# Kernel tuning notes

Hardware: AMD Instinct MI355X
Metric: run time of the kernel (lower is better)

Reference implementation:

```python
import jax, jax.numpy as jnp
import numpy as np

N = 50000   # nodes
E = 800000  # edges
F_IN, F_HID, F_OUT = 128, 96, 40


def setup_inputs() -> dict:
    key = jax.random.key(0)
    ks = jax.random.split(key, 9)
    x = jax.random.normal(ks[0], (N, F_IN), dtype=jnp.float32)
    edge_index = jax.random.randint(ks[1], (2, E), 0, N, dtype=jnp.int32)
    def lin(k, fi, fo):
        s = 1.0 / np.sqrt(fi)
        return jax.random.uniform(k, (fi, fo), jnp.float32, -s, s)
    W1 = lin(ks[2], F_IN, F_HID)
    b1 = jnp.zeros((F_HID,), jnp.float32)
    W2 = lin(ks[3], F_HID, F_HID)
    b2 = jnp.zeros((F_HID,), jnp.float32)
    Wout = lin(ks[4], F_HID, F_OUT)
    bout = jnp.zeros((F_OUT,), jnp.float32)
    return {"x": x, "edge_index": edge_index, "W1": W1, "b1": b1,
            "W2": W2, "b2": b2, "Wout": Wout, "bout": bout}


def _gcn_norm(edge_index, n):
    # add self-loops, symmetric degree normalization (PyG GCNConv default)
    loops = jnp.arange(n, dtype=edge_index.dtype)
    src = jnp.concatenate([edge_index[0], loops])
    dst = jnp.concatenate([edge_index[1], loops])
    deg = jax.ops.segment_sum(jnp.ones_like(dst, dtype=jnp.float32), dst,
                              num_segments=n)
    dinv = jnp.where(deg > 0, jax.lax.rsqrt(deg), 0.0)
    norm = dinv[src] * dinv[dst]   # [E+N]
    return src, dst, norm


def _gcn_layer(h, src, dst, norm, W, b, n):
    # linear transform, then normalized scatter-add aggregation, then bias
    h = h @ W                                 # [N, Fout]
    msg = h[src] * norm[:, None]              # gather + scale
    agg = jax.ops.segment_sum(msg, dst, num_segments=n)
    return agg + b


def reference(x, edge_index, W1, b1, W2, b2, Wout, bout):
    n = x.shape[0]
    src, dst, norm = _gcn_norm(edge_index, n)
    h = jax.nn.relu(_gcn_layer(x, src, dst, norm, W1, b1, n))
    h = jax.nn.relu(_gcn_layer(h, src, dst, norm, W2, b2, n))
    return h @ Wout + bout
```

## Files before the change

kernel.cpp:

```cpp
#include <hip/hip_runtime.h>
#include <hip/hip_fp16.h>

#define N_NODES 50000
#define N_EDGES 800000
#define F_INN   128
#define F_HID   96
#define F_OUTT  40

typedef _Float16 half8 __attribute__((ext_vector_type(8)));
typedef float    floatx4 __attribute__((ext_vector_type(4)));

template <int FI, typename TIN>
__device__ __forceinline__ void mfma_gemm_body(
        const TIN* __restrict__ X, const __half* __restrict__ BTg,
        float4* __restrict__ Th4, int n, int bx) {
    __shared__ __half BTl[96 * 136];
    __half* OUTl = BTl;
    int tid = threadIdx.x;
    {
        const int4* s = reinterpret_cast<const int4*>(BTg);
        int4* d = reinterpret_cast<int4*>(BTl);
        for (int i = tid; i < 96 * 136 / 8; i += 256) d[i] = s[i];
    }
    __syncthreads();

    int lane = tid & 63, w = tid >> 6;
    int lm = lane & 15, q = lane >> 4;
    int base = bx * 64 + w * 16;
    int node = base + lm;
    int nclamp = min(node, n - 1);
    const TIN* Xrow = X + (size_t)nclamp * FI;

    floatx4 cf[6];
    #pragma unroll
    for (int t = 0; t < 6; ++t) cf[t] = (floatx4){0.f, 0.f, 0.f, 0.f};

    constexpr int KS = FI / 32;
    #pragma unroll
    for (int ks = 0; ks < KS; ++ks) {
        half8 bv;
        if constexpr (sizeof(TIN) == 4) {
            const float4* xr = reinterpret_cast<const float4*>(Xrow + 32 * ks + q * 8);
            float4 f0 = xr[0], f1 = xr[1];
            union { half8 v; __half2 h[4]; } b;
            b.h[0] = __floats2half2_rn(f0.x, f0.y);
            b.h[1] = __floats2half2_rn(f0.z, f0.w);
            b.h[2] = __floats2half2_rn(f1.x, f1.y);
            b.h[3] = __floats2half2_rn(f1.z, f1.w);
            bv = b.v;
        } else {
            bv = *reinterpret_cast<const half8*>(Xrow + 32 * ks + q * 8);
        }
        #pragma unroll
        for (int t = 0; t < 6; ++t) {
            half8 a = *reinterpret_cast<const half8*>(
                &BTl[(t * 16 + lm) * 136 + q * 8 + 32 * ks]);
            cf[t] = __builtin_amdgcn_mfma_f32_16x16x32_f16(a, bv, cf[t], 0, 0, 0);
        }
    }

    __syncthreads();

    __half* orow = OUTl + (w * 16 + lm) * 104;
    #pragma unroll
    for (int t = 0; t < 6; ++t) {
        union { int2 i2; __half2 h[2]; } u;
        u.h[0] = __floats2half2_rn(cf[t][0], cf[t][1]);
        u.h[1] = __floats2half2_rn(cf[t][2], cf[t][3]);
        *reinterpret_cast<int2*>(&orow[t * 16 + q * 4]) = u.i2;
    }
    #pragma unroll
    for (int R = 0; R < 3; ++R) {
        int nl = lane >> 2, c = (lane & 3) + 4 * R;
        float4 v = *reinterpret_cast<const float4*>(&OUTl[(w * 16 + nl) * 104 + c * 8]);
        int gn = base + nl;
        if (gn < n) Th4[(size_t)gn * 12 + c] = v;
    }
}

__global__ __launch_bounds__(256) void count_gemm1_kernel(
        const int* __restrict__ dst, int* __restrict__ counts4, int* __restrict__ rank,
        int e, const float* __restrict__ X, const __half* __restrict__ BT1,
        float4* __restrict__ Th4, int n, int nCB) {
    if ((int)blockIdx.x < nCB) {
        int i = blockIdx.x * 512 + threadIdx.x;
        int j = i + 256;
        int di = 0, dj = 0, ri, rj;
        bool bi = i < e, bj = j < e;
        if (bi) di = dst[i];
        if (bj) dj = dst[j];
        if (bi) ri = atomicAdd(&counts4[di * 4 + (i & 3)], 1);
        if (bj) rj = atomicAdd(&counts4[dj * 4 + (j & 3)], 1);
        if (bi) rank[i] = ri;
        if (bj) rank[j] = rj;
    } else {
        mfma_gemm_body<F_INN, float>(X, BT1, Th4, n, blockIdx.x - nCB);
    }
}

template <int FI, typename TIN>
__global__ __launch_bounds__(256) void mfma_gemm_kernel(
        const TIN* __restrict__ X, const __half* __restrict__ BTg,
        float4* __restrict__ Th4, int n) {
    mfma_gemm_body<FI, TIN>(X, BTg, Th4, n, blockIdx.x);
}

__global__ void wt_kernel(const float* __restrict__ W1, const float* __restrict__ W2,
                          __half* __restrict__ BT1, __half* __restrict__ BT2) {
    int i = blockIdx.x * 256 + threadIdx.x;
    if (i < 96 * 128) {
        int j = i / 128, k = i - j * 128;
        BT1[j * 136 + k] = __float2half(W1[k * 96 + j]);
    } else if (i < 96 * 128 + 96 * 96) {
        int t = i - 96 * 128;
        int j = t / 96, k = t - j * 96;
        BT2[j * 136 + k] = __float2half(W2[k * 96 + j]);
    }
}

__global__ __launch_bounds__(1024) void scan_local_kernel(
        const int4* __restrict__ counts4, int* __restrict__ row_start,
        float* __restrict__ dinv, int* __restrict__ blk_sums, int n) {
    __shared__ int wave_sums[16];
    int tid = threadIdx.x, lane = tid & 63, wid = tid >> 6;
    int i = blockIdx.x * 1024 + tid;
    int v = 0;
    if (i < n) {
        int4 c = counts4[i];
        v = c.x + c.y + c.z + c.w;
    }
    int val = v;
    #pragma unroll
    for (int off = 1; off < 64; off <<= 1) {
        int u = __shfl_up(val, off, 64);
        if (lane >= off) val += u;
    }
    if (lane == 63) wave_sums[wid] = val;
    __syncthreads();
    if (wid == 0) {
        int w = (lane < 16) ? wave_sums[lane] : 0;
        #pragma unroll
        for (int off = 1; off < 16; off <<= 1) {
            int u = __shfl_up(w, off, 64);
            if (lane >= off) w += u;
        }
        if (lane < 16) wave_sums[lane] = w;
    }
    __syncthreads();
    int excl = ((wid == 0) ? 0 : wave_sums[wid - 1]) + (val - v);
    if (i < n) {
        row_start[i] = excl;
        dinv[i] = rsqrtf((float)(v + 1));
    }
    if (tid == 0) blk_sums[blockIdx.x] = wave_sums[15];
}

__global__ __launch_bounds__(1024) void scan_apply_kernel(
        int* __restrict__ row_start, const int* __restrict__ blk_sums,
        const int4* __restrict__ counts4, int4* __restrict__ base4, int n, int nblk) {
    __shared__ int s_my, s_tot;
    int tid = threadIdx.x;
    if (tid < 64) {
        int v = (tid < nblk) ? blk_sums[tid] : 0;
        int val = v;
        #pragma unroll
        for (int off = 1; off < 64; off <<= 1) {
            int u = __shfl_up(val, off, 64);
            if (tid >= off) val += u;
        }
        if (tid == (int)blockIdx.x) s_my = val - v;
        if (tid == 63) s_tot = val;
    }
    __syncthreads();
    int i = blockIdx.x * 1024 + tid;
    if (i < n) {
        int4 c = counts4[i];
        int b = row_start[i] + s_my;
        row_start[i] = b;
        base4[i] = make_int4(b, b + c.x, b + c.x + c.y, b + c.x + c.y + c.z);
    }
    if (blockIdx.x == 0 && tid == 0) row_start[n] = s_tot;
}

__global__ void fill_csr_kernel(const int* __restrict__ src, const int* __restrict__ dst,
                                const int* __restrict__ rank, const int* __restrict__ base4,
                                int* __restrict__ csr_src, int e) {
    int i = blockIdx.x * blockDim.x + threadIdx.x;
    if (i >= e) return;
    csr_src[base4[dst[i] * 4 + (i & 3)] + rank[i]] = src[i];
}

__global__ __launch_bounds__(256) void agg_kernel(
        const __half2* __restrict__ T, const int* __restrict__ row_start,
        const int* __restrict__ csr_src, const float* __restrict__ dinv,
        const float* __restrict__ bias, __half2* __restrict__ H, int n) {
    int lane = threadIdx.x & 63;
    int node = __builtin_amdgcn_readfirstlane(blockIdx.x * 4 + (threadIdx.x >> 6));
    if (node >= n) return;
    int fl = min(lane, 47);

    float dn = dinv[node];
    float2 self = __half22float2(T[(size_t)node * 48 + fl]);
    float accx = dn * self.x, accy = dn * self.y;

    int idx = row_start[node];
    int end = row_start[node + 1];
    for (; idx + 8 <= end; idx += 8) {
        int s[8];
        #pragma unroll
        for (int u = 0; u < 8; ++u) s[u] = csr_src[idx + u];
        float ws[8];
        #pragma unroll
        for (int u = 0; u < 8; ++u) ws[u] = dinv[s[u]];
        float2 f[8];
        #pragma unroll
        for (int u = 0; u < 8; ++u) f[u] = __half22float2(T[(size_t)s[u] * 48 + fl]);
        #pragma unroll
        for (int u = 0; u < 8; ++u) {
            accx = fmaf(ws[u], f[u].x, accx);
            accy = fmaf(ws[u], f[u].y, accy);
        }
    }
    for (; idx < end; ++idx) {
        int s = csr_src[idx];
        float w = dinv[s];
        float2 f = __half22float2(T[(size_t)s * 48 + fl]);
        accx = fmaf(w, f.x, accx);
        accy = fmaf(w, f.y, accy);
    }
    if (lane < 48) {
        float2 b = reinterpret_cast<const float2*>(bias)[lane];
        float ox = fmaxf(fmaf(dn, accx, b.x), 0.f);
        float oy = fmaxf(fmaf(dn, accy, b.y), 0.f);
        H[(size_t)node * 48 + lane] = __floats2half2_rn(ox, oy);
    }
}

__global__ __launch_bounds__(320) void gemm_out_kernel(
        const __half2* __restrict__ A, const float* __restrict__ W,
        const float* __restrict__ bias, float* __restrict__ C, int n) {
    __shared__ float Wlds[96 * 40];
    int tid = threadIdx.y * 10 + threadIdx.x;
    for (int i = tid; i < 96 * 10; i += 320)
        reinterpret_cast<float4*>(Wlds)[i] = reinterpret_cast<const float4*>(W)[i];
    __syncthreads();

    int j    = threadIdx.x * 4;
    int node = blockIdx.x * 32 + threadIdx.y;
    int nc   = min(node, n - 1);
    const __half2* Ah = A + (size_t)nc * 48;
    float4 acc = make_float4(0.f, 0.f, 0.f, 0.f);
    for (int k2 = 0; k2 < 48; k2 += 2) {
        float2 a01 = __half22float2(Ah[k2]);
        float2 a23 = __half22float2(Ah[k2 + 1]);
        int k = 2 * k2;
        float4 w0 = *reinterpret_cast<const float4*>(Wlds + (k + 0) * 40 + j);
        float4 w1 = *reinterpret_cast<const float4*>(Wlds + (k + 1) * 40 + j);
        float4 w2 = *reinterpret_cast<const float4*>(Wlds + (k + 2) * 40 + j);
        float4 w3 = *reinterpret_cast<const float4*>(Wlds + (k + 3) * 40 + j);
        acc.x += a01.x * w0.x + a01.y * w1.x + a23.x * w2.x + a23.y * w3.x;
        acc.y += a01.x * w0.y + a01.y * w1.y + a23.x * w2.y + a23.y * w3.y;
        acc.z += a01.x * w0.z + a01.y * w1.z + a23.x * w2.z + a23.y * w3.z;
        acc.w += a01.x * w0.w + a01.y * w1.w + a23.x * w2.w + a23.y * w3.w;
    }
    if (node < n) {
        float4 b = *reinterpret_cast<const float4*>(bias + j);
        acc.x += b.x; acc.y += b.y; acc.z += b.z; acc.w += b.w;
        *reinterpret_cast<float4*>(C + (size_t)node * 40 + j) = acc;
    }
}


extern "C" void kernel_launch(void* const* d_in, const int* in_sizes, int n_in,
                              void* d_out, int out_size, void* d_ws, size_t ws_size,
                              hipStream_t stream) {
    const float* x    = (const float*)d_in[0];
    const int*   ei   = (const int*)d_in[1];
    const float* W1   = (const float*)d_in[2];
    const float* b1   = (const float*)d_in[3];
    const float* W2   = (const float*)d_in[4];
    const float* b2   = (const float*)d_in[5];
    const float* Wout = (const float*)d_in[6];
    const float* bout = (const float*)d_in[7];
    float*       out  = (float*)d_out;

    const int* src = ei;
    const int* dst = ei + N_EDGES;

    char* ws = (char*)d_ws;
    size_t off = 0;
    auto alloc = [&](size_t bytes) {
        size_t o = off;
        off = (off + bytes + 511) & ~(size_t)511;
        return (void*)(ws + o);
    };
    int*     counts4   = (int*)    alloc((size_t)N_NODES * 4 * sizeof(int));
    int4*    base4     = (int4*)   alloc((size_t)N_NODES * sizeof(int4));
    int*     row_start = (int*)    alloc((N_NODES + 1) * sizeof(int));
    float*   dinv      = (float*)  alloc(N_NODES * sizeof(float));
    int*     blk_sums  = (int*)    alloc(64 * sizeof(int));
    int*     rank      = (int*)    alloc((size_t)N_EDGES * sizeof(int));
    int*     csr_src   = (int*)    alloc((size_t)N_EDGES * sizeof(int));
    __half*  BT1       = (__half*) alloc((size_t)96 * 136 * sizeof(__half));
    __half*  BT2       = (__half*) alloc((size_t)96 * 136 * sizeof(__half));
    __half2* Th        = (__half2*)alloc((size_t)N_NODES * 48 * sizeof(__half2));
    __half2* Hh        = (__half2*)alloc((size_t)N_NODES * 48 * sizeof(__half2));

    const int NSCAN = (N_NODES + 1023) / 1024;
    const int CB2   = (N_EDGES + 511) / 512;
    const int FB    = (N_EDGES + 255) / 256;
    const int GB    = (N_NODES + 63) / 64;

    hipMemsetAsync(counts4, 0, (size_t)N_NODES * 4 * sizeof(int), stream);
    wt_kernel<<<(96 * 128 + 96 * 96 + 255) / 256, 256, 0, stream>>>(W1, W2, BT1, BT2);

    count_gemm1_kernel<<<CB2 + GB, 256, 0, stream>>>(
        dst, counts4, rank, N_EDGES, x, BT1, (float4*)Th, N_NODES, CB2);

    scan_local_kernel<<<NSCAN, 1024, 0, stream>>>(
        (const int4*)counts4, row_start, dinv, blk_sums, N_NODES);
    scan_apply_kernel<<<NSCAN, 1024, 0, stream>>>(
        row_start, blk_sums, (const int4*)counts4, base4, N_NODES, NSCAN);
    fill_csr_kernel<<<FB, 256, 0, stream>>>(
        src, dst, rank, (const int*)base4, csr_src, N_EDGES);

    agg_kernel<<<(N_NODES + 3) / 4, 256, 0, stream>>>(
        Th, row_start, csr_src, dinv, b1, Hh, N_NODES);

    mfma_gemm_kernel<F_HID, __half><<<GB, 256, 0, stream>>>(
        (const __half*)Hh, BT2, (float4*)Th, N_NODES);
    agg_kernel<<<(N_NODES + 3) / 4, 256, 0, stream>>>(
        Th, row_start, csr_src, dinv, b2, Hh, N_NODES);

    gemm_out_kernel<<<(N_NODES + 31) / 32, dim3(10, 32), 0, stream>>>(
        Hh, Wout, bout, out, N_NODES);
}
```

Measured before the change: 230.1 us.

## Build CSR with atomic cursors instead of stored per-edge ranks

The count kernel no longer records a per-edge rank from its atomic; instead the scan writes per-node sub-bucket cursors and the fill kernel claims slots by atomically incrementing those cursors, with four edges per thread. This removes the rank array write and read (about 6.4 MB of traffic) at the cost of a second pass of atomics in the fill stage. Edge order within a node's row becomes nondeterministic, which can change floating-point summation order in aggregation.

```diff
diff --git a/kernel.cpp b/kernel.cpp
--- a/kernel.cpp
+++ b/kernel.cpp
@@ -79,20 +79,18 @@
 }
 
 __global__ __launch_bounds__(256) void count_gemm1_kernel(
-        const int* __restrict__ dst, int* __restrict__ counts4, int* __restrict__ rank,
+        const int* __restrict__ dst, int* __restrict__ counts4,
         int e, const float* __restrict__ X, const __half* __restrict__ BT1,
         float4* __restrict__ Th4, int n, int nCB) {
     if ((int)blockIdx.x < nCB) {
         int i = blockIdx.x * 512 + threadIdx.x;
         int j = i + 256;
-        int di = 0, dj = 0, ri, rj;
+        int di = 0, dj = 0;
         bool bi = i < e, bj = j < e;
         if (bi) di = dst[i];
         if (bj) dj = dst[j];
-        if (bi) ri = atomicAdd(&counts4[di * 4 + (i & 3)], 1);
-        if (bj) rj = atomicAdd(&counts4[dj * 4 + (j & 3)], 1);
-        if (bi) rank[i] = ri;
-        if (bj) rank[j] = rj;
+        if (bi) atomicAdd(&counts4[di * 4 + (i & 3)], 1);
+        if (bj) atomicAdd(&counts4[dj * 4 + (j & 3)], 1);
     } else {
         mfma_gemm_body<F_INN, float>(X, BT1, Th4, n, blockIdx.x - nCB);
     }
@@ -157,7 +155,7 @@
 
 __global__ __launch_bounds__(1024) void scan_apply_kernel(
         int* __restrict__ row_start, const int* __restrict__ blk_sums,
-        const int4* __restrict__ counts4, int4* __restrict__ base4, int n, int nblk) {
+        const int4* __restrict__ counts4, int4* __restrict__ cursor4, int n, int nblk) {
     __shared__ int s_my, s_tot;
     int tid = threadIdx.x;
     if (tid < 64) {
@@ -177,17 +175,30 @@
         int4 c = counts4[i];
         int b = row_start[i] + s_my;
         row_start[i] = b;
-        base4[i] = make_int4(b, b + c.x, b + c.x + c.y, b + c.x + c.y + c.z);
+        cursor4[i] = make_int4(b, b + c.x, b + c.x + c.y, b + c.x + c.y + c.z);
     }
     if (blockIdx.x == 0 && tid == 0) row_start[n] = s_tot;
 }
 
-__global__ void fill_csr_kernel(const int* __restrict__ src, const int* __restrict__ dst,
-                                const int* __restrict__ rank, const int* __restrict__ base4,
-                                int* __restrict__ csr_src, int e) {
-    int i = blockIdx.x * blockDim.x + threadIdx.x;
-    if (i >= e) return;
-    csr_src[base4[dst[i] * 4 + (i & 3)] + rank[i]] = src[i];
+__global__ __launch_bounds__(256) void fill_csr_kernel(
+        const int* __restrict__ src, const int* __restrict__ dst,
+        int* __restrict__ cursor4, int* __restrict__ csr_src, int e) {
+    int i0 = blockIdx.x * 1024 + threadIdx.x;
+    int sh = i0 & 3;
+    int d[4], s[4], p[4];
+    bool b[4];
+    #pragma unroll
+    for (int u = 0; u < 4; ++u) {
+        int i = i0 + u * 256;
+        b[u] = i < e;
+        if (b[u]) { d[u] = dst[i]; s[u] = src[i]; }
+    }
+    #pragma unroll
+    for (int u = 0; u < 4; ++u)
+        if (b[u]) p[u] = atomicAdd(&cursor4[d[u] * 4 + sh], 1);
+    #pragma unroll
+    for (int u = 0; u < 4; ++u)
+        if (b[u]) csr_src[p[u]] = s[u];
 }
 
 __global__ __launch_bounds__(256) void agg_kernel(
@@ -295,11 +306,10 @@
         return (void*)(ws + o);
     };
     int*     counts4   = (int*)    alloc((size_t)N_NODES * 4 * sizeof(int));
-    int4*    base4     = (int4*)   alloc((size_t)N_NODES * sizeof(int4));
+    int4*    cursor4   = (int4*)   alloc((size_t)N_NODES * sizeof(int4));
     int*     row_start = (int*)    alloc((N_NODES + 1) * sizeof(int));
     float*   dinv      = (float*)  alloc(N_NODES * sizeof(float));
     int*     blk_sums  = (int*)    alloc(64 * sizeof(int));
-    int*     rank      = (int*)    alloc((size_t)N_EDGES * sizeof(int));
     int*     csr_src   = (int*)    alloc((size_t)N_EDGES * sizeof(int));
     __half*  BT1       = (__half*) alloc((size_t)96 * 136 * sizeof(__half));
     __half*  BT2       = (__half*) alloc((size_t)96 * 136 * sizeof(__half));
@@ -308,21 +318,21 @@
 
     const int NSCAN = (N_NODES + 1023) / 1024;
     const int CB2   = (N_EDGES + 511) / 512;
-    const int FB    = (N_EDGES + 255) / 256;
+    const int FB4   = (N_EDGES + 1023) / 1024;
     const int GB    = (N_NODES + 63) / 64;
 
     hipMemsetAsync(counts4, 0, (size_t)N_NODES * 4 * sizeof(int), stream);
     wt_kernel<<<(96 * 128 + 96 * 96 + 255) / 256, 256, 0, stream>>>(W1, W2, BT1, BT2);
 
     count_gemm1_kernel<<<CB2 + GB, 256, 0, stream>>>(
-        dst, counts4, rank, N_EDGES, x, BT1, (float4*)Th, N_NODES, CB2);
+        dst, counts4, N_EDGES, x, BT1, (float4*)Th, N_NODES, CB2);
 
     scan_local_kernel<<<NSCAN, 1024, 0, stream>>>(
         (const int4*)counts4, row_start, dinv, blk_sums, N_NODES);
     scan_apply_kernel<<<NSCAN, 1024, 0, stream>>>(
-        row_start, blk_sums, (const int4*)counts4, base4, N_NODES, NSCAN);
-    fill_csr_kernel<<<FB, 256, 0, stream>>>(
-        src, dst, rank, (const int*)base4, csr_src, N_EDGES);
+        row_start, blk_sums, (const int4*)counts4, cursor4, N_NODES, NSCAN);
+    fill_csr_kernel<<<FB4, 256, 0, stream>>>(
+        src, dst, (int*)cursor4, csr_src, N_EDGES);
 
     agg_kernel<<<(N_NODES + 3) / 4, 256, 0, stream>>>(
         Th, row_start, csr_src, dinv, b1, Hh, N_NODES);
```

After: 255.6 us. +11.1%, slower.
